# Performance work log

Hardware: AMD Instinct MI355X
Metric: run time of the kernel (lower is better)

## Reference

```python
import jax, jax.numpy as jnp
import numpy as np

# Fixed production-scale sizes (equal-sized graphs so unbatch == reshape)
B, NQ, ND = 64, 32, 512     # graph pairs, query nodes/graph, data nodes/graph
DIN, D, K = 64, 128, 16     # GCN_in_size, GCN_out_size, NTN_k
DEG = 8                     # average degree


def _gcn(x, src, dst, W, b):
    """GCNConv with self loops + symmetric normalization (PyG semantics)."""
    N = x.shape[0]
    loop = jnp.arange(N)
    s = jnp.concatenate([src, loop])
    t = jnp.concatenate([dst, loop])
    deg = jax.ops.segment_sum(jnp.ones_like(t, x.dtype), t, num_segments=N)
    dinv = jnp.where(deg > 0, deg ** -0.5, 0.0)
    norm = (dinv[s] * dinv[t])[:, None]
    h = x @ W
    return jax.ops.segment_sum(h[s] * norm, t, num_segments=N) + b


def _three_gcn(x, ei, W1, b1, W2, b2, W3, b3):
    src, dst = ei[0], ei[1]
    h1 = jax.nn.relu(_gcn(x, src, dst, W1, b1))
    h2 = jax.nn.relu(_gcn(h1, src, dst, W2, b2))
    h3 = jax.nn.relu(_gcn(h2, src, dst, W3, b3))
    return h1, h2, h3


def _level(q, d, Wn, Vn, bn, cw, cb):
    """att_layer + NTN + elementwise mult + 1x1 conv + softmax over data nodes.
    q: [B,NQ,D], d: [B,ND,D] -> (softmaxed map [B,NQ,ND], raw map, he [B,K,NQ,ND])."""
    att = jax.nn.softmax(jnp.einsum('bqd,bnd->bqn', q, d) / jnp.sqrt(jnp.float32(D)), axis=-1)
    qW = jnp.einsum('bqd,kde->bkqe', q, Wn)           # [B,K,NQ,D]
    bil = jnp.einsum('bkqe,bne->bkqn', qW, d)          # [B,K,NQ,ND]
    lq = jnp.einsum('kd,bqd->bkq', Vn[:, :D], q)[:, :, :, None]
    ld = jnp.einsum('kd,bnd->bkn', Vn[:, D:], d)[:, :, None, :]
    he = jax.nn.sigmoid(bil + lq + ld + bn[None, :, None, None]) * att[:, None]
    e_raw = jnp.einsum('k,bkqn->bqn', cw, he) + cb     # 1x1 Conv2d(K->1)
    return jax.nn.softmax(e_raw, axis=-1), e_raw, he


def reference(x_d, edge_index_d, x_q, edge_index_q, batch_index_d, batch_index_q,
              W1, b1, W2, b2, W3, b3,
              Wn1, Vn1, bn1, cw1, cb1,
              Wn2, Vn2, bn2, cw2, cb2,
              Wn3, Vn3, bn3, cw3, cb3,
              w_end, b_end):
    d1, d2, d3 = _three_gcn(x_d, edge_index_d, W1, b1, W2, b2, W3, b3)
    q1, q2, q3 = _three_gcn(x_q, edge_index_q, W1, b1, W2, b2, W3, b3)
    # unbatch: batch indices are sorted with equal graph sizes -> reshape
    d1, d2, d3 = (t.reshape(B, ND, D) for t in (d1, d2, d3))
    q1, q2, q3 = (t.reshape(B, NQ, D) for t in (q1, q2, q3))
    e1, _, he1 = _level(q1, d1, Wn1, Vn1, bn1, cw1, cb1)
    _, e2raw, he2 = _level(q2, d2, Wn2, Vn2, bn2, cw2, cb2)
    e3, _, he3 = _level(q3, d3, Wn3, Vn3, bn3, cw3, cb3)
    # Faithful to source quirks: the zip unpack `e1,e2,e3,h1,h2,h1` rebinds h1 to
    # he_3 (he_1 is never used, he_3 appears twice) and end2 enters the concat
    # PRE-softmax (the softmaxed version was assigned to unused `nd2`).
    stack = jnp.concatenate([e1[:, None], e2raw[:, None], e3[:, None], he3, he2, he3], axis=1)
    out = jnp.einsum('c,bcqn->bqn', w_end, stack) + b_end  # con_end 1x1 conv + squeeze
    return jax.nn.softmax(out, axis=-1)                    # softmax over data nodes


def setup_inputs() -> dict:
    key = jax.random.key(0)
    k = jax.random.split(key, 40)
    n = jax.random.normal
    Nd, Nq = B * ND, B * NQ
    Ed, Eq = Nd * DEG, Nq * DEG
    gid_d = jnp.repeat(jnp.arange(B), ND * DEG)
    gid_q = jnp.repeat(jnp.arange(B), NQ * DEG)
    inp = {
        'x_d': n(k[0], (Nd, DIN), jnp.float32),
        'x_q': n(k[1], (Nq, DIN), jnp.float32),
        'edge_index_d': jnp.stack([jax.random.randint(k[2], (Ed,), 0, ND) + gid_d * ND,
                                   jax.random.randint(k[3], (Ed,), 0, ND) + gid_d * ND]),
        'edge_index_q': jnp.stack([jax.random.randint(k[4], (Eq,), 0, NQ) + gid_q * NQ,
                                   jax.random.randint(k[5], (Eq,), 0, NQ) + gid_q * NQ]),
        'batch_index_d': jnp.repeat(jnp.arange(B), ND),
        'batch_index_q': jnp.repeat(jnp.arange(B), NQ),
        'W1': n(k[6], (DIN, D), jnp.float32) / np.sqrt(DIN), 'b1': jnp.zeros((D,), jnp.float32),
        'W2': n(k[7], (D, D), jnp.float32) / np.sqrt(D), 'b2': jnp.zeros((D,), jnp.float32),
        'W3': n(k[8], (D, D), jnp.float32) / np.sqrt(D), 'b3': jnp.zeros((D,), jnp.float32),
    }
    for i, l in enumerate(('1', '2', '3')):
        inp['Wn' + l] = n(k[10 + 4 * i], (K, D, D), jnp.float32) / np.sqrt(D)
        inp['Vn' + l] = n(k[11 + 4 * i], (K, 2 * D), jnp.float32) / np.sqrt(2 * D)
        inp['bn' + l] = jnp.zeros((K,), jnp.float32)
        inp['cw' + l] = n(k[12 + 4 * i], (K,), jnp.float32) / np.sqrt(K)
        inp['cb' + l] = jnp.zeros((1,), jnp.float32)
    inp['w_end'] = n(k[25], (3 * K + 3,), jnp.float32) / np.sqrt(3 * K + 3)
    inp['b_end'] = jnp.zeros((1,), jnp.float32)
    return inp
```

## Files before the change

### kernel.cpp

```cpp
#include <hip/hip_runtime.h>
#include <math.h>

namespace {
constexpr int cB  = 64;
constexpr int cNQ = 32;
constexpr int cND = 512;
constexpr int cNd = cB * cND;
constexpr int cNq = cB * cNQ;
constexpr int cEd = cNd * 8;
constexpr int cEq = cNq * 8;
constexpr int LD_STRIDE = 516;
constexpr int NB_CVT = 2188, NB_T2BF = 808, NB_CNT = (cEd + cEq) / 256;
constexpr int NB_FILL = (cEd + cEq) / 256;
}

#define F4C(p) (*(const float4*)(p))
#define F4W(p) (*(float4*)(p))

typedef __attribute__((ext_vector_type(8))) __bf16 bf16x8;
typedef __attribute__((ext_vector_type(4))) float floatx4;

__device__ __forceinline__ ushort f2bf(float f) {
  union { float f; unsigned u; } v;
  v.f = f;
  unsigned u = v.u;
  return (ushort)((u + 0x7fffu + ((u >> 16) & 1u)) >> 16);
}
__device__ __forceinline__ float bf2f(ushort u) {
  union { unsigned u; float f; } v;
  v.u = ((unsigned)u) << 16;
  return v.f;
}
__device__ __forceinline__ float4 us4f4(ushort4 u) {
  return make_float4(bf2f(u.x), bf2f(u.y), bf2f(u.z), bf2f(u.w));
}
__device__ __forceinline__ ushort4 f4us4(float4 f) {
  ushort4 o;
  o.x = f2bf(f.x); o.y = f2bf(f.y); o.z = f2bf(f.z); o.w = f2bf(f.w);
  return o;
}
__device__ __forceinline__ float fexp2(float x) {
#if __has_builtin(__builtin_amdgcn_exp2f)
  return __builtin_amdgcn_exp2f(x);
#else
  return exp2f(x);
#endif
}
__device__ __forceinline__ float frcp(float x) {
#if __has_builtin(__builtin_amdgcn_rcpf)
  return __builtin_amdgcn_rcpf(x);
#else
  return 1.0f / x;
#endif
}
__device__ __forceinline__ float fsigmoid(float z) {
  return frcp(1.0f + fexp2(z * -1.4426950408889634f));
}
__device__ __forceinline__ float fexp(float x) { return fexp2(x * 1.4426950408889634f); }

__device__ __forceinline__ int swz_g(int j) { return (((j >> 3) & 7) << 3) | (j & 7); }

__global__ __launch_bounds__(256) void k_front(
    const float* __restrict__ xd, const float* __restrict__ xq,
    const float* __restrict__ v0, const float* __restrict__ v1,
    const float* __restrict__ v2, ushort* __restrict__ oxd, ushort* __restrict__ oxq,
    ushort* __restrict__ ov0, ushort* __restrict__ ov1, ushort* __restrict__ ov2,
    const float* __restrict__ W1, const float* __restrict__ W2,
    const float* __restrict__ W3, const float* __restrict__ Wn0,
    const float* __restrict__ Wn1, const float* __restrict__ Wn2,
    ushort* __restrict__ o1, ushort* __restrict__ o2, ushort* __restrict__ o3,
    ushort* __restrict__ on0, ushort* __restrict__ on1, ushort* __restrict__ on2,
    const int* __restrict__ dst_d, const int* __restrict__ dst_q,
    int* __restrict__ cnt_d, int* __restrict__ cnt_q) {
  __shared__ float tile[32][33];
  int blk = blockIdx.x, tid = threadIdx.x;
  if (blk < NB_CVT) {
    const float* src;
    ushort* dst;
    int i;
    if (blk < 2048) { src = xd; dst = oxd; i = blk * 256 + tid; }
    else if (blk < 2176) { src = xq; dst = oxq; i = (blk - 2048) * 256 + tid; }
    else if (blk < 2180) { src = v0; dst = ov0; i = (blk - 2176) * 256 + tid; }
    else if (blk < 2184) { src = v1; dst = ov1; i = (blk - 2180) * 256 + tid; }
    else { src = v2; dst = ov2; i = (blk - 2184) * 256 + tid; }
    *(ushort4*)(dst + (size_t)i * 4) = f4us4(F4C(src + (size_t)i * 4));
  } else if (blk < NB_CVT + NB_T2BF) {
    int b5 = blk - NB_CVT;
    const float* in;
    ushort* out;
    int R, C, bt, t;
    if (b5 < 8)        { in = W1;  out = o1;  R = 64;  C = 128; bt = 0; t = b5; }
    else if (b5 < 24)  { in = W2;  out = o2;  R = 128; C = 128; bt = 0; t = b5 - 8; }
    else if (b5 < 40)  { in = W3;  out = o3;  R = 128; C = 128; bt = 0; t = b5 - 24; }
    else if (b5 < 296) { in = Wn0; out = on0; R = 128; C = 128; bt = (b5 - 40) >> 4;  t = (b5 - 40) & 15; }
    else if (b5 < 552) { in = Wn1; out = on1; R = 128; C = 128; bt = (b5 - 296) >> 4; t = (b5 - 296) & 15; }
    else               { in = Wn2; out = on2; R = 128; C = 128; bt = (b5 - 552) >> 4; t = (b5 - 552) & 15; }
    int tilesC = C >> 5;
    int tr = t / tilesC, tc = t - tr * tilesC;
    int tx = tid & 31, ty = tid >> 5;
    const float* ib = in + (size_t)bt * R * C;
    ushort* ob = out + (size_t)bt * R * C;
#pragma unroll
    for (int i = 0; i < 4; ++i)
      tile[ty + i * 8][tx] = ib[(tr * 32 + ty + i * 8) * C + tc * 32 + tx];
    __syncthreads();
#pragma unroll
    for (int i = 0; i < 4; ++i)
      ob[(size_t)(tc * 32 + ty + i * 8) * R + tr * 32 + tx] = f2bf(tile[tx][ty + i * 8]);
  } else {
    int i = (blk - NB_CVT - NB_T2BF) * 256 + tid;
    if (i < cEd) atomicAdd(&cnt_d[dst_d[i]], 1);
    else atomicAdd(&cnt_q[dst_q[i - cEd]], 1);
  }
}

__global__ __launch_bounds__(512) void k_scan_dinv(
    const int* __restrict__ cnt_d, const int* __restrict__ cnt_q,
    int* __restrict__ rp_d, int* __restrict__ rp_q,
    float* __restrict__ dinv_d, float* __restrict__ dinv_q) {
  __shared__ int sh[512];
  int blk = blockIdx.x, tid = threadIdx.x;
  if (blk < 64) {
    int v = cnt_d[blk * 512 + tid];
    sh[tid] = v;
    __syncthreads();
    for (int off = 1; off < 512; off <<= 1) {
      int t = (tid >= off) ? sh[tid - off] : 0;
      __syncthreads();
      sh[tid] += t;
      __syncthreads();
    }
    rp_d[blk * 512 + tid] = blk * 4096 + sh[tid] - v;
  } else if (blk < 68) {
    int g = (blk - 64) * 16 + (tid >> 5);
    int lane32 = tid & 31;
    int v = cnt_q[g * 32 + lane32];
    int incl = v;
#pragma unroll
    for (int off = 1; off < 32; off <<= 1) {
      int t = __shfl_up(incl, off, 32);
      if (lane32 >= off) incl += t;
    }
    rp_q[g * 32 + lane32] = g * 256 + incl - v;
  } else {
    int i = (blk - 68) * 512 + tid;
    if (i < cNd) dinv_d[i] = 1.0f / sqrtf((float)(cnt_d[i] + 1));
    else dinv_q[i - cNd] = 1.0f / sqrtf((float)(cnt_q[i - cNd] + 1));
  }
}

__global__ __launch_bounds__(256) void k_fill_gemm1(
    const int* __restrict__ src_d, const int* __restrict__ dst_d,
    const int* __restrict__ src_q, const int* __restrict__ dst_q,
    const int* __restrict__ rp_d, const int* __restrict__ rp_q,
    int* __restrict__ cur_d, int* __restrict__ cur_q, int* __restrict__ col_d,
    int* __restrict__ col_q, const ushort* __restrict__ xdbf,
    const ushort* __restrict__ xqbf, const ushort* __restrict__ w1T,
    const float* __restrict__ dinv_d, const float* __restrict__ dinv_q,
    ushort* __restrict__ htmp) {
  int blk = blockIdx.x, tid = threadIdx.x;
  if (blk < NB_FILL) {
    int i = blk * 256 + tid;
    if (i < cEd) {
      int d = dst_d[i];
      int p = atomicAdd(&cur_d[d], 1);
      col_d[rp_d[d] + p] = src_d[i];
    } else {
      int j = i - cEd;
      int d = dst_q[j];
      int p = atomicAdd(&cur_q[d], 1);
      col_q[rp_q[d] + p] = src_q[j];
    }
    return;
  }
  int blk2 = blk - NB_FILL;
  int wave = tid >> 6, lane = tid & 63;
  int col = lane & 15, quad = lane >> 4;
  bool isQ = blk2 >= 512;
  int node0;
  if (isQ) node0 = (blk2 - 512) * 64;
  else node0 = swz_g(blk2) * 512 + (blk2 >> 6) * 64;
  int mloc = node0 + wave * 16;
  const ushort* X = isQ ? xqbf : xdbf;
  const float* dv = isQ ? dinv_q : dinv_d;
  size_t hbase = isQ ? (size_t)cNd : 0;
  floatx4 acc[8];
#pragma unroll
  for (int ct = 0; ct < 8; ++ct)
#pragma unroll
    for (int r = 0; r < 4; ++r) acc[ct][r] = 0.0f;
#pragma unroll
  for (int kc = 0; kc < 2; ++kc) {
    bf16x8 a = *(const bf16x8*)(X + (size_t)(mloc + col) * 64 + kc * 32 + quad * 8);
#pragma unroll
    for (int ct = 0; ct < 8; ++ct) {
      bf16x8 b = *(const bf16x8*)(w1T + (size_t)(ct * 16 + col) * 64 + kc * 32 + quad * 8);
      acc[ct] = __builtin_amdgcn_mfma_f32_16x16x32_bf16(a, b, acc[ct], 0, 0, 0);
    }
  }
  float sc[4];
#pragma unroll
  for (int r = 0; r < 4; ++r) sc[r] = dv[mloc + quad * 4 + r];
#pragma unroll
  for (int ct = 0; ct < 8; ++ct)
#pragma unroll
    for (int r = 0; r < 4; ++r)
      htmp[(hbase + mloc + quad * 4 + r) * 128 + ct * 16 + col] = f2bf(acc[ct][r] * sc[r]);
}

__global__ __launch_bounds__(256) void gmn_gather_merged(
    const ushort* __restrict__ htmp, const int* __restrict__ rp_d,
    const int* __restrict__ cnt_d, const int* __restrict__ col_d,
    const float* __restrict__ dinv_d, const int* __restrict__ rp_q,
    const int* __restrict__ cnt_q, const int* __restrict__ col_q,
    const float* __restrict__ dinv_q, const float* __restrict__ bias,
    ushort* __restrict__ dbf, ushort* __restrict__ qbf) {
  int blk = blockIdx.x, tid = threadIdx.x;
  bool isQ = blk >= 4096;
  int node;
  if (isQ) {
    int j = blk - 4096;
    node = swz_g(j) * 32 + (j >> 6) * 8 + (tid >> 5);
  } else {
    node = swz_g(blk) * 512 + (blk >> 6) * 8 + (tid >> 5);
  }
  int l = tid & 31;
  const ushort* hs = htmp + (isQ ? (size_t)cNd * 128 : 0);
  const int* rp = isQ ? rp_q : rp_d;
  const int* cnt = isQ ? cnt_q : cnt_d;
  const int* col = isQ ? col_q : col_d;
  const float* dinv = isQ ? dinv_q : dinv_d;
  ushort* outp = isQ ? qbf : dbf;
  int c = cnt[node], s0 = rp[node];
  float dt = dinv[node];
  float4 acc = us4f4(*(const ushort4*)(hs + (size_t)node * 128 + l * 4));
  int cm = c < 32 ? c : 32;
  for (int j0 = 0; j0 < cm; j0 += 8) {
    int ss[8];
    ushort4 v[8];
#pragma unroll
    for (int t = 0; t < 8; ++t) {
      int jj = j0 + t;
      ss[t] = (jj < cm) ? col[s0 + jj] : -1;
    }
#pragma unroll
    for (int t = 0; t < 8; ++t)
      if (ss[t] >= 0) v[t] = *(const ushort4*)(hs + (size_t)ss[t] * 128 + l * 4);
#pragma unroll
    for (int t = 0; t < 8; ++t) {
      if (ss[t] >= 0) {
        float4 f = us4f4(v[t]);
        acc.x += f.x; acc.y += f.y; acc.z += f.z; acc.w += f.w;
      }
    }
  }
  for (int j = 32; j < c; ++j) {
    int s = col[s0 + j];
    float4 f = us4f4(*(const ushort4*)(hs + (size_t)s * 128 + l * 4));
    acc.x += f.x; acc.y += f.y; acc.z += f.z; acc.w += f.w;
  }
  float4 bv = F4C(bias + l * 4);
  float4 r;
  r.x = fmaxf(acc.x * dt + bv.x, 0.0f);
  r.y = fmaxf(acc.y * dt + bv.y, 0.0f);
  r.z = fmaxf(acc.z * dt + bv.z, 0.0f);
  r.w = fmaxf(acc.w * dt + bv.w, 0.0f);
  *(ushort4*)(outp + (size_t)node * 128 + l * 4) = f4us4(r);
}

__global__ __launch_bounds__(256) void gmn_qw(const ushort* __restrict__ qbf,
                                              const ushort* __restrict__ wnT,
                                              ushort* __restrict__ qw) {
  int blk = blockIdx.x, tid = threadIdx.x;
  int wave = tid >> 6, lane = tid & 63;
  int col = lane & 15, quad = lane >> 4;
  int b = swz_g(blk), k = blk >> 6;
  int et0 = wave * 2;
  floatx4 acc[2][2];
#pragma unroll
  for (int qt = 0; qt < 2; ++qt)
#pragma unroll
    for (int ei = 0; ei < 2; ++ei)
#pragma unroll
      for (int r = 0; r < 4; ++r) acc[qt][ei][r] = 0.0f;
#pragma unroll
  for (int kc = 0; kc < 4; ++kc) {
    bf16x8 a0 = *(const bf16x8*)(qbf + (size_t)(b * 32 + col) * 128 + kc * 32 + quad * 8);
    bf16x8 a1 = *(const bf16x8*)(qbf + (size_t)(b * 32 + 16 + col) * 128 + kc * 32 + quad * 8);
#pragma unroll
    for (int ei = 0; ei < 2; ++ei) {
      bf16x8 bf = *(const bf16x8*)(wnT + (size_t)(k * 128 + (et0 + ei) * 16 + col) * 128 +
                                   kc * 32 + quad * 8);
      acc[0][ei] = __builtin_amdgcn_mfma_f32_16x16x32_bf16(a0, bf, acc[0][ei], 0, 0, 0);
      acc[1][ei] = __builtin_amdgcn_mfma_f32_16x16x32_bf16(a1, bf, acc[1][ei], 0, 0, 0);
    }
  }
#pragma unroll
  for (int qt = 0; qt < 2; ++qt)
#pragma unroll
    for (int ei = 0; ei < 2; ++ei)
#pragma unroll
      for (int r = 0; r < 4; ++r)
        qw[((size_t)(b * 16 + k) << 12) + (qt * 16 + quad * 4 + r) * 128 +
           (et0 + ei) * 16 + col] = f2bf(acc[qt][ei][r]);
}

__global__ __launch_bounds__(512, 2) void k_level_gemm(
    const ushort* __restrict__ qbf, const ushort* __restrict__ dbf,
    const ushort* __restrict__ qw, const ushort* __restrict__ vnbf,
    const float* __restrict__ bn, const float* __restrict__ cw,
    const float* __restrict__ w_end, const float* __restrict__ b_end,
    int o1, int o2, int hasF, int do_sm, int mode, int widx,
    float* __restrict__ accb, float* __restrict__ out,
    const ushort* __restrict__ gWT, const float* __restrict__ dinv_d,
    const float* __restrict__ dinv_q, ushort* __restrict__ htmp) {
  __shared__ float s_ld[16 * LD_STRIDE];
  __shared__ float s_lq[16 * 16];
  __shared__ float s_red[16 * 8];
  int tid = threadIdx.x;
  int wave = tid >> 6, lane = tid & 63;
  int col = lane & 15, quad = lane >> 4;

  if (blockIdx.x >= 128) {
    int gblk = blockIdx.x - 128;
    bool isQ = gblk >= 256;
    int node0;
    if (isQ) node0 = (gblk - 256) * 128;
    else node0 = swz_g(gblk) * 512 + (gblk >> 6) * 128;
    int mloc = node0 + wave * 16;
    const ushort* X = isQ ? qbf : dbf;
    const float* dv = isQ ? dinv_q : dinv_d;
    size_t hbase = isQ ? (size_t)cNd : 0;
    floatx4 acc[8];
#pragma unroll
    for (int ct = 0; ct < 8; ++ct)
#pragma unroll
      for (int r = 0; r < 4; ++r) acc[ct][r] = 0.0f;
#pragma unroll
    for (int kc = 0; kc < 4; ++kc) {
      bf16x8 a = *(const bf16x8*)(X + (size_t)(mloc + col) * 128 + kc * 32 + quad * 8);
#pragma unroll
      for (int ct = 0; ct < 8; ++ct) {
        bf16x8 b = *(const bf16x8*)(gWT + (size_t)(ct * 16 + col) * 128 + kc * 32 + quad * 8);
        acc[ct] = __builtin_amdgcn_mfma_f32_16x16x32_bf16(a, b, acc[ct], 0, 0, 0);
      }
    }
    float sc[4];
#pragma unroll
    for (int r = 0; r < 4; ++r) sc[r] = dv[mloc + quad * 4 + r];
#pragma unroll
    for (int ct = 0; ct < 8; ++ct)
#pragma unroll
      for (int r = 0; r < 4; ++r)
        htmp[(hbase + mloc + quad * 4 + r) * 128 + ct * 16 + col] = f2bf(acc[ct][r] * sc[r]);
    return;
  }

  int b = swz_g(blockIdx.x & 63);
  int qh = blockIdx.x >> 6;
  int n0 = wave * 64;

  bf16x8 bfr[4][4];
#pragma unroll
  for (int s = 0; s < 4; ++s)
#pragma unroll
    for (int kc = 0; kc < 4; ++kc)
      bfr[s][kc] = *(const bf16x8*)(dbf + ((size_t)(b * 512 + n0 + s * 16 + col) << 7) +
                                    kc * 32 + quad * 8);
  bf16x8 aq[4];
#pragma unroll
  for (int kc = 0; kc < 4; ++kc)
    aq[kc] = *(const bf16x8*)(qbf + (size_t)(b * 32 + qh * 16 + col) * 128 +
                              kc * 32 + quad * 8);

  floatx4 att[4];
#pragma unroll
  for (int s = 0; s < 4; ++s)
#pragma unroll
    for (int r = 0; r < 4; ++r) att[s][r] = 0.0f;
#pragma unroll
  for (int kc = 0; kc < 4; ++kc)
#pragma unroll
    for (int s = 0; s < 4; ++s)
      att[s] = __builtin_amdgcn_mfma_f32_16x16x32_bf16(aq[kc], bfr[s][kc], att[s], 0, 0, 0);
  const float sc = 0.088388347648318440550f;
#pragma unroll
  for (int s = 0; s < 4; ++s)
#pragma unroll
    for (int r = 0; r < 4; ++r) att[s][r] *= sc;

  {
    bf16x8 vn2[4];
#pragma unroll
    for (int kc = 0; kc < 4; ++kc)
      vn2[kc] = *(const bf16x8*)(vnbf + col * 256 + 128 + kc * 32 + quad * 8);
#pragma unroll
    for (int s = 0; s < 4; ++s) {
      floatx4 lda;
#pragma unroll
      for (int r = 0; r < 4; ++r) lda[r] = 0.0f;
#pragma unroll
      for (int kc = 0; kc < 4; ++kc)
        lda = __builtin_amdgcn_mfma_f32_16x16x32_bf16(bfr[s][kc], vn2[kc], lda, 0, 0, 0);
#pragma unroll
      for (int r = 0; r < 4; ++r)
        s_ld[col * LD_STRIDE + n0 + s * 16 + quad * 4 + r] = lda[r];
    }
  }
  if (wave == 0) {
    bf16x8 vn1[4];
#pragma unroll
    for (int kc = 0; kc < 4; ++kc)
      vn1[kc] = *(const bf16x8*)(vnbf + col * 256 + kc * 32 + quad * 8);
    floatx4 lqa;
#pragma unroll
    for (int r = 0; r < 4; ++r) lqa[r] = 0.0f;
#pragma unroll
    for (int kc = 0; kc < 4; ++kc)
      lqa = __builtin_amdgcn_mfma_f32_16x16x32_bf16(aq[kc], vn1[kc], lqa, 0, 0, 0);
#pragma unroll
    for (int r = 0; r < 4; ++r) s_lq[col * 16 + quad * 4 + r] = lqa[r];
  }
  __syncthreads();

  float red[4], M[4];
#pragma unroll
  for (int r = 0; r < 4; ++r) {
    float m = fmaxf(fmaxf(att[0][r], att[1][r]), fmaxf(att[2][r], att[3][r]));
#pragma unroll
    for (int o = 1; o < 16; o <<= 1) m = fmaxf(m, __shfl_xor(m, o, 64));
    red[r] = m;
  }
  if (col == 0)
#pragma unroll
    for (int r = 0; r < 4; ++r) s_red[(quad * 4 + r) * 8 + wave] = red[r];
  __syncthreads();
#pragma unroll
  for (int r = 0; r < 4; ++r) {
    float m = s_red[(quad * 4 + r) * 8];
#pragma unroll
    for (int w = 1; w < 8; ++w) m = fmaxf(m, s_red[(quad * 4 + r) * 8 + w]);
    M[r] = m;
  }
  __syncthreads();
#pragma unroll
  for (int s = 0; s < 4; ++s)
#pragma unroll
    for (int r = 0; r < 4; ++r) att[s][r] = fexp(att[s][r] - M[r]);
#pragma unroll
  for (int r = 0; r < 4; ++r) {
    float m = att[0][r] + att[1][r] + att[2][r] + att[3][r];
#pragma unroll
    for (int o = 1; o < 16; o <<= 1) m += __shfl_xor(m, o, 64);
    red[r] = m;
  }
  if (col == 0)
#pragma unroll
    for (int r = 0; r < 4; ++r) s_red[(quad * 4 + r) * 8 + wave] = red[r];
  __syncthreads();
#pragma unroll
  for (int r = 0; r < 4; ++r) {
    float m = s_red[(quad * 4 + r) * 8];
#pragma unroll
    for (int w = 1; w < 8; ++w) m += s_red[(quad * 4 + r) * 8 + w];
    M[r] = frcp(m);
  }
  __syncthreads();
#pragma unroll
  for (int s = 0; s < 4; ++s)
#pragma unroll
    for (int r = 0; r < 4; ++r) att[s][r] *= M[r];

  floatx4 eacc[4], facc[4];
#pragma unroll
  for (int s = 0; s < 4; ++s)
#pragma unroll
    for (int r = 0; r < 4; ++r) { eacc[s][r] = 0.0f; facc[s][r] = 0.0f; }

#pragma unroll 4
  for (int k = 0; k < 16; ++k) {
    const ushort* qk = qw + ((size_t)(b * 16 + k) << 12) + (qh * 16 + col) * 128 + quad * 8;
    bf16x8 a0 = *(const bf16x8*)(qk);
    bf16x8 a1 = *(const bf16x8*)(qk + 32);
    bf16x8 a2 = *(const bf16x8*)(qk + 64);
    bf16x8 a3 = *(const bf16x8*)(qk + 96);
    floatx4 bil[4];
#pragma unroll
    for (int s = 0; s < 4; ++s) {
#pragma unroll
      for (int r = 0; r < 4; ++r) bil[s][r] = 0.0f;
      bil[s] = __builtin_amdgcn_mfma_f32_16x16x32_bf16(a0, bfr[s][0], bil[s], 0, 0, 0);
      bil[s] = __builtin_amdgcn_mfma_f32_16x16x32_bf16(a1, bfr[s][1], bil[s], 0, 0, 0);
      bil[s] = __builtin_amdgcn_mfma_f32_16x16x32_bf16(a2, bfr[s][2], bil[s], 0, 0, 0);
      bil[s] = __builtin_amdgcn_mfma_f32_16x16x32_bf16(a3, bfr[s][3], bil[s], 0, 0, 0);
    }
    float bnk = bn[k], cwk = cw[k];
    float wkk = 0.0f;
    if (hasF) {
      wkk = w_end[o1 + k];
      if (o2 >= 0) wkk += w_end[o2 + k];
    }
    float lqv[4];
#pragma unroll
    for (int r = 0; r < 4; ++r) lqv[r] = s_lq[k * 16 + quad * 4 + r] + bnk;
#pragma unroll
    for (int s = 0; s < 4; ++s) {
      float ldv = s_ld[k * LD_STRIDE + n0 + s * 16 + col];
#pragma unroll
      for (int r = 0; r < 4; ++r) {
        float sg = fsigmoid(bil[s][r] + lqv[r] + ldv);
        eacc[s][r] += cwk * sg;
        facc[s][r] += wkk * sg;
      }
    }
  }

#pragma unroll
  for (int s = 0; s < 4; ++s)
#pragma unroll
    for (int r = 0; r < 4; ++r) {
      eacc[s][r] *= att[s][r];
      facc[s][r] *= att[s][r];
    }
  if (do_sm) {
#pragma unroll
    for (int r = 0; r < 4; ++r) {
      float m = fmaxf(fmaxf(eacc[0][r], eacc[1][r]), fmaxf(eacc[2][r], eacc[3][r]));
#pragma unroll
      for (int o = 1; o < 16; o <<= 1) m = fmaxf(m, __shfl_xor(m, o, 64));
      red[r] = m;
    }
    if (col == 0)
#pragma unroll
      for (int r = 0; r < 4; ++r) s_red[(quad * 4 + r) * 8 + wave] = red[r];
    __syncthreads();
#pragma unroll
    for (int r = 0; r < 4; ++r) {
      float m = s_red[(quad * 4 + r) * 8];
#pragma unroll
      for (int w = 1; w < 8; ++w) m = fmaxf(m, s_red[(quad * 4 + r) * 8 + w]);
      M[r] = m;
    }
    __syncthreads();
#pragma unroll
    for (int s = 0; s < 4; ++s)
#pragma unroll
      for (int r = 0; r < 4; ++r) eacc[s][r] = fexp(eacc[s][r] - M[r]);
#pragma unroll
    for (int r = 0; r < 4; ++r) {
      float m = eacc[0][r] + eacc[1][r] + eacc[2][r] + eacc[3][r];
#pragma unroll
      for (int o = 1; o < 16; o <<= 1) m += __shfl_xor(m, o, 64);
      red[r] = m;
    }
    if (col == 0)
#pragma unroll
      for (int r = 0; r < 4; ++r) s_red[(quad * 4 + r) * 8 + wave] = red[r];
    __syncthreads();
#pragma unroll
    for (int r = 0; r < 4; ++r) {
      float m = s_red[(quad * 4 + r) * 8];
#pragma unroll
      for (int w = 1; w < 8; ++w) m += s_red[(quad * 4 + r) * 8 + w];
      M[r] = frcp(m);
    }
    __syncthreads();
#pragma unroll
    for (int s = 0; s < 4; ++s)
#pragma unroll
      for (int r = 0; r < 4; ++r) eacc[s][r] *= M[r];
  }
  float w = w_end[widx];
#pragma unroll
  for (int s = 0; s < 4; ++s)
#pragma unroll
    for (int r = 0; r < 4; ++r) eacc[s][r] = w * eacc[s][r] + (hasF ? facc[s][r] : 0.0f);

  if (mode == 0) {
#pragma unroll
    for (int s = 0; s < 4; ++s)
#pragma unroll
      for (int r = 0; r < 4; ++r)
        accb[((size_t)(b * 32 + qh * 16 + quad * 4 + r) << 9) + n0 + s * 16 + col] =
            eacc[s][r];
  } else if (mode == 1) {
#pragma unroll
    for (int s = 0; s < 4; ++s)
#pragma unroll
      for (int r = 0; r < 4; ++r)
        accb[((size_t)(b * 32 + qh * 16 + quad * 4 + r) << 9) + n0 + s * 16 + col] +=
            eacc[s][r];
  } else {
    float be = b_end[0];
#pragma unroll
    for (int s = 0; s < 4; ++s)
#pragma unroll
      for (int r = 0; r < 4; ++r)
        eacc[s][r] += accb[((size_t)(b * 32 + qh * 16 + quad * 4 + r) << 9) +
                           n0 + s * 16 + col] + be;
#pragma unroll
    for (int r = 0; r < 4; ++r) {
      float m = fmaxf(fmaxf(eacc[0][r], eacc[1][r]), fmaxf(eacc[2][r], eacc[3][r]));
#pragma unroll
      for (int o = 1; o < 16; o <<= 1) m = fmaxf(m, __shfl_xor(m, o, 64));
      red[r] = m;
    }
    if (col == 0)
#pragma unroll
      for (int r = 0; r < 4; ++r) s_red[(quad * 4 + r) * 8 + wave] = red[r];
    __syncthreads();
#pragma unroll
    for (int r = 0; r < 4; ++r) {
      float m = s_red[(quad * 4 + r) * 8];
#pragma unroll
      for (int w2 = 1; w2 < 8; ++w2) m = fmaxf(m, s_red[(quad * 4 + r) * 8 + w2]);
      M[r] = m;
    }
    __syncthreads();
#pragma unroll
    for (int s = 0; s < 4; ++s)
#pragma unroll
      for (int r = 0; r < 4; ++r) eacc[s][r] = fexp(eacc[s][r] - M[r]);
#pragma unroll
    for (int r = 0; r < 4; ++r) {
      float m = eacc[0][r] + eacc[1][r] + eacc[2][r] + eacc[3][r];
#pragma unroll
      for (int o = 1; o < 16; o <<= 1) m += __shfl_xor(m, o, 64);
      red[r] = m;
    }
    if (col == 0)
#pragma unroll
      for (int r = 0; r < 4; ++r) s_red[(quad * 4 + r) * 8 + wave] = red[r];
    __syncthreads();
#pragma unroll
    for (int r = 0; r < 4; ++r) {
      float m = s_red[(quad * 4 + r) * 8];
#pragma unroll
      for (int w2 = 1; w2 < 8; ++w2) m += s_red[(quad * 4 + r) * 8 + w2];
      M[r] = frcp(m);
    }
#pragma unroll
    for (int s = 0; s < 4; ++s)
#pragma unroll
      for (int r = 0; r < 4; ++r)
        out[((size_t)(b * 32 + qh * 16 + quad * 4 + r) << 9) + n0 + s * 16 + col] =
            eacc[s][r] * M[r];
  }
}

extern "C" void kernel_launch(void* const* d_in, const int* in_sizes, int n_in,
                              void* d_out, int out_size, void* d_ws, size_t ws_size,
                              hipStream_t stream) {
  (void)in_sizes; (void)n_in; (void)out_size; (void)ws_size;
  const float* x_d = (const float*)d_in[0];
  const float* x_q = (const float*)d_in[1];
  const int* ei_d = (const int*)d_in[2];
  const int* ei_q = (const int*)d_in[3];
  const float* W1 = (const float*)d_in[6];
  const float* b1 = (const float*)d_in[7];
  const float* W2 = (const float*)d_in[8];
  const float* b2 = (const float*)d_in[9];
  const float* W3 = (const float*)d_in[10];
  const float* b3 = (const float*)d_in[11];
  const float* Wn[3] = {(const float*)d_in[12], (const float*)d_in[17], (const float*)d_in[22]};
  const float* Vn[3] = {(const float*)d_in[13], (const float*)d_in[18], (const float*)d_in[23]};
  const float* bn[3] = {(const float*)d_in[14], (const float*)d_in[19], (const float*)d_in[24]};
  const float* cw[3] = {(const float*)d_in[15], (const float*)d_in[20], (const float*)d_in[25]};
  const float* w_end = (const float*)d_in[27];
  const float* b_end = (const float*)d_in[28];
  float* out = (float*)d_out;

  char* wsp = (char*)d_ws;
  auto alloc = [&](size_t nbytes) {
    void* p = (void*)wsp;
    wsp += (nbytes + 255) & ~(size_t)255;
    return p;
  };
  int* cnt_d = (int*)alloc(cNd * 4);
  int* cnt_q = (int*)alloc(cNq * 4);
  int* cur_d = (int*)alloc(cNd * 4);
  int* cur_q = (int*)alloc(cNq * 4);
  float* dinv_d = (float*)alloc(cNd * 4);
  float* dinv_q = (float*)alloc(cNq * 4);
  int* rp_d = (int*)alloc(cNd * 4);
  int* rp_q = (int*)alloc(cNq * 4);
  int* col_d = (int*)alloc((size_t)cEd * 4);
  int* col_q = (int*)alloc((size_t)cEq * 4);
  ushort* xdbf = (ushort*)alloc((size_t)cNd * 64 * 2);
  ushort* xqbf = (ushort*)alloc((size_t)cNq * 64 * 2);
  ushort* w1T = (ushort*)alloc(128 * 64 * 2);
  ushort* w2T = (ushort*)alloc(128 * 128 * 2);
  ushort* w3T = (ushort*)alloc(128 * 128 * 2);
  ushort* wnT[3];
  for (int l = 0; l < 3; ++l) wnT[l] = (ushort*)alloc((size_t)16 * 128 * 128 * 2);
  ushort* vnbf[3];
  for (int l = 0; l < 3; ++l) vnbf[l] = (ushort*)alloc(16 * 256 * 2);
  ushort* htmp = (ushort*)alloc((size_t)(cNd + cNq) * 128 * 2);
  ushort* dbf = (ushort*)alloc((size_t)cNd * 128 * 2);
  ushort* qbf[3];
  for (int l = 0; l < 3; ++l) qbf[l] = (ushort*)alloc((size_t)cNq * 128 * 2);
  float* accb = (float*)alloc((size_t)cB * cNQ * cND * 4);
  ushort* qwbuf = (ushort*)alloc((size_t)cB * 16 * 32 * 128 * 2);

  const int* src_d = ei_d;
  const int* dst_d = ei_d + cEd;
  const int* src_q = ei_q;
  const int* dst_q = ei_q + cEq;

  hipMemsetAsync(cnt_d, 0, (size_t)2 * (cNd + cNq) * 4, stream);

  k_front<<<NB_CVT + NB_T2BF + NB_CNT, 256, 0, stream>>>(
      x_d, x_q, Vn[0], Vn[1], Vn[2], xdbf, xqbf, vnbf[0], vnbf[1], vnbf[2], W1, W2,
      W3, Wn[0], Wn[1], Wn[2], w1T, w2T, w3T, wnT[0], wnT[1], wnT[2], dst_d, dst_q,
      cnt_d, cnt_q);

  k_scan_dinv<<<136, 512, 0, stream>>>(cnt_d, cnt_q, rp_d, rp_q, dinv_d, dinv_q);

  k_fill_gemm1<<<NB_FILL + 544, 256, 0, stream>>>(
      src_d, dst_d, src_q, dst_q, rp_d, rp_q, cur_d, cur_q, col_d, col_q, xdbf, xqbf,
      w1T, dinv_d, dinv_q, htmp);

  const float* bias[3] = {b1, b2, b3};
  const ushort* nextWT[3] = {w2T, w3T, nullptr};
  const int o1s[3] = {0, 19, 3};
  const int o2s[3] = {-1, -1, 35};
  const int hasF[3] = {0, 1, 1};
  const int dosms[3] = {1, 0, 1};
  const int modes[3] = {0, 1, 2};

  for (int l = 0; l < 3; ++l) {
    gmn_gather_merged<<<(cNd + cNq) / 8, 256, 0, stream>>>(
        htmp, rp_d, cnt_d, col_d, dinv_d, rp_q, cnt_q, col_q, dinv_q, bias[l], dbf,
        qbf[l]);
    gmn_qw<<<1024, 256, 0, stream>>>(qbf[l], wnT[l], qwbuf);
    int grid = (l < 2) ? (128 + 272) : 128;
    k_level_gemm<<<grid, 512, 0, stream>>>(
        qbf[l], dbf, qwbuf, vnbf[l], bn[l], cw[l], w_end, b_end, o1s[l], o2s[l],
        hasF[l], dosms[l], modes[l], l, accb, out, nextWT[l], dinv_d, dinv_q, htmp);
  }
}
```

Baseline: 300.2 us.

## Build per-graph CSR in shared memory and fuse query gather with QW GEMM

CSR construction (count, scan, dinv, fill) now runs per graph inside the front kernel using shared-memory atomics. This drops the memset, the scan kernel and the global-atomic fill pass, and gemm1 becomes its own kernel. Per level, the query-node gather is merged into the qW GEMM: each block aggregates one graph's 32 query nodes into swizzled LDS and multiplies them against all K Wn slices, which removes one launch per level. The cost is that the QW work runs on only 64 blocks, each doing 16 K-slices serially, so parallelism drops.

```diff
diff --git a/kernel.cpp b/kernel.cpp
--- a/kernel.cpp
+++ b/kernel.cpp
@@ -10,8 +10,9 @@
 constexpr int cEd = cNd * 8;
 constexpr int cEq = cNq * 8;
 constexpr int LD_STRIDE = 516;
-constexpr int NB_CVT = 2188, NB_T2BF = 808, NB_CNT = (cEd + cEq) / 256;
-constexpr int NB_FILL = (cEd + cEq) / 256;
+constexpr int NB_CVT = 2188, NB_T2BF = 808;
+constexpr int NB_CSRD = 64;
+constexpr int NB_CSRQ = 8;
 }
 
 #define F4C(p) (*(const float4*)(p))
@@ -60,7 +61,7 @@
 
 __device__ __forceinline__ int swz_g(int j) { return (((j >> 3) & 7) << 3) | (j & 7); }
 
-__global__ __launch_bounds__(256) void k_front(
+__global__ __launch_bounds__(256) void k_front_csr(
     const float* __restrict__ xd, const float* __restrict__ xq,
     const float* __restrict__ v0, const float* __restrict__ v1,
     const float* __restrict__ v2, ushort* __restrict__ oxd, ushort* __restrict__ oxq,
@@ -70,9 +71,16 @@
     const float* __restrict__ Wn1, const float* __restrict__ Wn2,
     ushort* __restrict__ o1, ushort* __restrict__ o2, ushort* __restrict__ o3,
     ushort* __restrict__ on0, ushort* __restrict__ on1, ushort* __restrict__ on2,
-    const int* __restrict__ dst_d, const int* __restrict__ dst_q,
-    int* __restrict__ cnt_d, int* __restrict__ cnt_q) {
+    const int* __restrict__ src_d, const int* __restrict__ dst_d,
+    const int* __restrict__ src_q, const int* __restrict__ dst_q,
+    int* __restrict__ cnt_d, int* __restrict__ cnt_q,
+    int* __restrict__ rp_d, int* __restrict__ rp_q,
+    float* __restrict__ dinv_d, float* __restrict__ dinv_q,
+    int* __restrict__ col_d, int* __restrict__ col_q) {
   __shared__ float tile[32][33];
+  __shared__ int s_cnt[512];
+  __shared__ int s_base[512];
+  __shared__ int s_cur[512];
   int blk = blockIdx.x, tid = threadIdx.x;
   if (blk < NB_CVT) {
     const float* src;
@@ -107,73 +115,82 @@
 #pragma unroll
     for (int i = 0; i < 4; ++i)
       ob[(size_t)(tc * 32 + ty + i * 8) * R + tr * 32 + tx] = f2bf(tile[tx][ty + i * 8]);
+  } else if (blk < NB_CVT + NB_T2BF + NB_CSRD) {
+    int g = blk - (NB_CVT + NB_T2BF);
+    const int* dstg = dst_d + g * 4096;
+    const int* srcg = src_d + g * 4096;
+    int nbase = g * 512;
+    s_cnt[tid] = 0; s_cnt[tid + 256] = 0;
+    __syncthreads();
+    for (int e = tid; e < 4096; e += 256) atomicAdd(&s_cnt[dstg[e] - nbase], 1);
+    __syncthreads();
+    int c0 = s_cnt[tid], c1 = s_cnt[tid + 256];
+    s_base[tid] = c0; s_base[tid + 256] = c1;
+    __syncthreads();
+    for (int off = 1; off < 512; off <<= 1) {
+      int a = (tid >= off) ? s_base[tid - off] : 0;
+      int b = (tid + 256 >= off) ? s_base[tid + 256 - off] : 0;
+      __syncthreads();
+      s_base[tid] += a; s_base[tid + 256] += b;
+      __syncthreads();
+    }
+    int e0 = s_base[tid] - c0, e1 = s_base[tid + 256] - c1;
+    s_base[tid] = e0; s_base[tid + 256] = e1;
+    s_cur[tid] = 0; s_cur[tid + 256] = 0;
+    cnt_d[nbase + tid] = c0;
+    cnt_d[nbase + tid + 256] = c1;
+    rp_d[nbase + tid] = g * 4096 + e0;
+    rp_d[nbase + tid + 256] = g * 4096 + e1;
+    dinv_d[nbase + tid] = 1.0f / sqrtf((float)(c0 + 1));
+    dinv_d[nbase + tid + 256] = 1.0f / sqrtf((float)(c1 + 1));
+    __syncthreads();
+    for (int e = tid; e < 4096; e += 256) {
+      int d = dstg[e] - nbase;
+      int p = atomicAdd(&s_cur[d], 1);
+      col_d[g * 4096 + s_base[d] + p] = srcg[e];
+    }
   } else {
-    int i = (blk - NB_CVT - NB_T2BF) * 256 + tid;
-    if (i < cEd) atomicAdd(&cnt_d[dst_d[i]], 1);
-    else atomicAdd(&cnt_q[dst_q[i - cEd]], 1);
-  }
-}
-
-__global__ __launch_bounds__(512) void k_scan_dinv(
-    const int* __restrict__ cnt_d, const int* __restrict__ cnt_q,
-    int* __restrict__ rp_d, int* __restrict__ rp_q,
-    float* __restrict__ dinv_d, float* __restrict__ dinv_q) {
-  __shared__ int sh[512];
-  int blk = blockIdx.x, tid = threadIdx.x;
-  if (blk < 64) {
-    int v = cnt_d[blk * 512 + tid];
-    sh[tid] = v;
-    __syncthreads();
-    for (int off = 1; off < 512; off <<= 1) {
-      int t = (tid >= off) ? sh[tid - off] : 0;
-      __syncthreads();
-      sh[tid] += t;
-      __syncthreads();
-    }
-    rp_d[blk * 512 + tid] = blk * 4096 + sh[tid] - v;
-  } else if (blk < 68) {
-    int g = (blk - 64) * 16 + (tid >> 5);
-    int lane32 = tid & 31;
-    int v = cnt_q[g * 32 + lane32];
+    int qb = blk - (NB_CVT + NB_T2BF + NB_CSRD);
+    int lg = tid >> 5, lane32 = tid & 31;
+    int g = qb * 8 + lg;
+    const int* dstg = dst_q + g * 256;
+    const int* srcg = src_q + g * 256;
+    int nbase = g * 32;
+    s_cnt[tid] = 0;
+    __syncthreads();
+#pragma unroll
+    for (int j = 0; j < 8; ++j)
+      atomicAdd(&s_cnt[lg * 32 + (dstg[lane32 + j * 32] - nbase)], 1);
+    __syncthreads();
+    int v = s_cnt[tid];
     int incl = v;
 #pragma unroll
     for (int off = 1; off < 32; off <<= 1) {
       int t = __shfl_up(incl, off, 32);
       if (lane32 >= off) incl += t;
     }
-    rp_q[g * 32 + lane32] = g * 256 + incl - v;
-  } else {
-    int i = (blk - 68) * 512 + tid;
-    if (i < cNd) dinv_d[i] = 1.0f / sqrtf((float)(cnt_d[i] + 1));
-    else dinv_q[i - cNd] = 1.0f / sqrtf((float)(cnt_q[i - cNd] + 1));
-  }
-}
-
-__global__ __launch_bounds__(256) void k_fill_gemm1(
-    const int* __restrict__ src_d, const int* __restrict__ dst_d,
-    const int* __restrict__ src_q, const int* __restrict__ dst_q,
-    const int* __restrict__ rp_d, const int* __restrict__ rp_q,
-    int* __restrict__ cur_d, int* __restrict__ cur_q, int* __restrict__ col_d,
-    int* __restrict__ col_q, const ushort* __restrict__ xdbf,
-    const ushort* __restrict__ xqbf, const ushort* __restrict__ w1T,
-    const float* __restrict__ dinv_d, const float* __restrict__ dinv_q,
-    ushort* __restrict__ htmp) {
-  int blk = blockIdx.x, tid = threadIdx.x;
-  if (blk < NB_FILL) {
-    int i = blk * 256 + tid;
-    if (i < cEd) {
-      int d = dst_d[i];
-      int p = atomicAdd(&cur_d[d], 1);
-      col_d[rp_d[d] + p] = src_d[i];
-    } else {
-      int j = i - cEd;
-      int d = dst_q[j];
-      int p = atomicAdd(&cur_q[d], 1);
-      col_q[rp_q[d] + p] = src_q[j];
-    }
-    return;
-  }
-  int blk2 = blk - NB_FILL;
+    int excl = incl - v;
+    cnt_q[nbase + lane32] = v;
+    rp_q[nbase + lane32] = g * 256 + excl;
+    dinv_q[nbase + lane32] = 1.0f / sqrtf((float)(v + 1));
+    s_base[tid] = excl;
+    s_cur[tid] = 0;
+    __syncthreads();
+#pragma unroll
+    for (int j = 0; j < 8; ++j) {
+      int e = lane32 + j * 32;
+      int d = dstg[e] - nbase;
+      int p = atomicAdd(&s_cur[lg * 32 + d], 1);
+      col_q[g * 256 + s_base[lg * 32 + d] + p] = srcg[e];
+    }
+  }
+}
+
+__global__ __launch_bounds__(256) void k_gemm1(
+    const ushort* __restrict__ xdbf, const ushort* __restrict__ xqbf,
+    const ushort* __restrict__ w1T, const float* __restrict__ dinv_d,
+    const float* __restrict__ dinv_q, ushort* __restrict__ htmp) {
+  int blk2 = blockIdx.x, tid = threadIdx.x;
   int wave = tid >> 6, lane = tid & 63;
   int col = lane & 15, quad = lane >> 4;
   bool isQ = blk2 >= 512;
@@ -208,101 +225,140 @@
       htmp[(hbase + mloc + quad * 4 + r) * 128 + ct * 16 + col] = f2bf(acc[ct][r] * sc[r]);
 }
 
-__global__ __launch_bounds__(256) void gmn_gather_merged(
+__global__ __launch_bounds__(256) void k_gather_qw(
     const ushort* __restrict__ htmp, const int* __restrict__ rp_d,
     const int* __restrict__ cnt_d, const int* __restrict__ col_d,
     const float* __restrict__ dinv_d, const int* __restrict__ rp_q,
     const int* __restrict__ cnt_q, const int* __restrict__ col_q,
     const float* __restrict__ dinv_q, const float* __restrict__ bias,
-    ushort* __restrict__ dbf, ushort* __restrict__ qbf) {
+    ushort* __restrict__ dbf, ushort* __restrict__ qbf,
+    const ushort* __restrict__ wnT, ushort* __restrict__ qw) {
+  __shared__ ushort q_s[32 * 128];
   int blk = blockIdx.x, tid = threadIdx.x;
-  bool isQ = blk >= 4096;
-  int node;
-  if (isQ) {
-    int j = blk - 4096;
-    node = swz_g(j) * 32 + (j >> 6) * 8 + (tid >> 5);
-  } else {
-    node = swz_g(blk) * 512 + (blk >> 6) * 8 + (tid >> 5);
-  }
-  int l = tid & 31;
-  const ushort* hs = htmp + (isQ ? (size_t)cNd * 128 : 0);
-  const int* rp = isQ ? rp_q : rp_d;
-  const int* cnt = isQ ? cnt_q : cnt_d;
-  const int* col = isQ ? col_q : col_d;
-  const float* dinv = isQ ? dinv_q : dinv_d;
-  ushort* outp = isQ ? qbf : dbf;
-  int c = cnt[node], s0 = rp[node];
-  float dt = dinv[node];
-  float4 acc = us4f4(*(const ushort4*)(hs + (size_t)node * 128 + l * 4));
-  int cm = c < 32 ? c : 32;
-  for (int j0 = 0; j0 < cm; j0 += 8) {
-    int ss[8];
-    ushort4 v[8];
-#pragma unroll
-    for (int t = 0; t < 8; ++t) {
-      int jj = j0 + t;
-      ss[t] = (jj < cm) ? col[s0 + jj] : -1;
-    }
-#pragma unroll
-    for (int t = 0; t < 8; ++t)
-      if (ss[t] >= 0) v[t] = *(const ushort4*)(hs + (size_t)ss[t] * 128 + l * 4);
-#pragma unroll
-    for (int t = 0; t < 8; ++t) {
-      if (ss[t] >= 0) {
-        float4 f = us4f4(v[t]);
-        acc.x += f.x; acc.y += f.y; acc.z += f.z; acc.w += f.w;
+  if (blk >= 64) {
+    int j = blk - 64;
+    int node = swz_g(j) * 512 + (j >> 6) * 8 + (tid >> 5);
+    int l = tid & 31;
+    int c = cnt_d[node], s0 = rp_d[node];
+    float dt = dinv_d[node];
+    float4 acc = us4f4(*(const ushort4*)(htmp + (size_t)node * 128 + l * 4));
+    int cm = c < 32 ? c : 32;
+    for (int j0 = 0; j0 < cm; j0 += 8) {
+      int ss[8];
+      ushort4 v[8];
+#pragma unroll
+      for (int t = 0; t < 8; ++t) {
+        int jj = j0 + t;
+        ss[t] = (jj < cm) ? col_d[s0 + jj] : -1;
       }
-    }
-  }
-  for (int j = 32; j < c; ++j) {
-    int s = col[s0 + j];
-    float4 f = us4f4(*(const ushort4*)(hs + (size_t)s * 128 + l * 4));
-    acc.x += f.x; acc.y += f.y; acc.z += f.z; acc.w += f.w;
-  }
-  float4 bv = F4C(bias + l * 4);
-  float4 r;
-  r.x = fmaxf(acc.x * dt + bv.x, 0.0f);
-  r.y = fmaxf(acc.y * dt + bv.y, 0.0f);
-  r.z = fmaxf(acc.z * dt + bv.z, 0.0f);
-  r.w = fmaxf(acc.w * dt + bv.w, 0.0f);
-  *(ushort4*)(outp + (size_t)node * 128 + l * 4) = f4us4(r);
-}
-
-__global__ __launch_bounds__(256) void gmn_qw(const ushort* __restrict__ qbf,
-                                              const ushort* __restrict__ wnT,
-                                              ushort* __restrict__ qw) {
-  int blk = blockIdx.x, tid = threadIdx.x;
+#pragma unroll
+      for (int t = 0; t < 8; ++t)
+        if (ss[t] >= 0) v[t] = *(const ushort4*)(htmp + (size_t)ss[t] * 128 + l * 4);
+#pragma unroll
+      for (int t = 0; t < 8; ++t) {
+        if (ss[t] >= 0) {
+          float4 f = us4f4(v[t]);
+          acc.x += f.x; acc.y += f.y; acc.z += f.z; acc.w += f.w;
+        }
+      }
+    }
+    for (int j2 = 32; j2 < c; ++j2) {
+      int s = col_d[s0 + j2];
+      float4 f = us4f4(*(const ushort4*)(htmp + (size_t)s * 128 + l * 4));
+      acc.x += f.x; acc.y += f.y; acc.z += f.z; acc.w += f.w;
+    }
+    float4 bv = F4C(bias + l * 4);
+    float4 r;
+    r.x = fmaxf(acc.x * dt + bv.x, 0.0f);
+    r.y = fmaxf(acc.y * dt + bv.y, 0.0f);
+    r.z = fmaxf(acc.z * dt + bv.z, 0.0f);
+    r.w = fmaxf(acc.w * dt + bv.w, 0.0f);
+    *(ushort4*)(dbf + (size_t)node * 128 + l * 4) = f4us4(r);
+    return;
+  }
+  int b = blk;
+  {
+    int n = tid >> 3, seg = tid & 7, d0 = seg * 16;
+    int node = b * 32 + n;
+    int c = cnt_q[node], s0 = rp_q[node];
+    float dt = dinv_q[node];
+    const ushort* hq = htmp + (size_t)cNd * 128;
+    const ushort* own = hq + (size_t)node * 128 + d0;
+    float4 a0 = us4f4(*(const ushort4*)(own));
+    float4 a1 = us4f4(*(const ushort4*)(own + 4));
+    float4 a2 = us4f4(*(const ushort4*)(own + 8));
+    float4 a3 = us4f4(*(const ushort4*)(own + 12));
+    for (int j2 = 0; j2 < c; ++j2) {
+      int s = col_q[s0 + j2];
+      const ushort* rr = hq + (size_t)s * 128 + d0;
+      float4 f0 = us4f4(*(const ushort4*)(rr));
+      float4 f1 = us4f4(*(const ushort4*)(rr + 4));
+      float4 f2 = us4f4(*(const ushort4*)(rr + 8));
+      float4 f3 = us4f4(*(const ushort4*)(rr + 12));
+      a0.x += f0.x; a0.y += f0.y; a0.z += f0.z; a0.w += f0.w;
+      a1.x += f1.x; a1.y += f1.y; a1.z += f1.z; a1.w += f1.w;
+      a2.x += f2.x; a2.y += f2.y; a2.z += f2.z; a2.w += f2.w;
+      a3.x += f3.x; a3.y += f3.y; a3.z += f3.z; a3.w += f3.w;
+    }
+    float4 bv0 = F4C(bias + d0), bv1 = F4C(bias + d0 + 4);
+    float4 bv2 = F4C(bias + d0 + 8), bv3 = F4C(bias + d0 + 12);
+    float4 r0, r1, r2, r3;
+    r0.x = fmaxf(a0.x * dt + bv0.x, 0.0f); r0.y = fmaxf(a0.y * dt + bv0.y, 0.0f);
+    r0.z = fmaxf(a0.z * dt + bv0.z, 0.0f); r0.w = fmaxf(a0.w * dt + bv0.w, 0.0f);
+    r1.x = fmaxf(a1.x * dt + bv1.x, 0.0f); r1.y = fmaxf(a1.y * dt + bv1.y, 0.0f);
+    r1.z = fmaxf(a1.z * dt + bv1.z, 0.0f); r1.w = fmaxf(a1.w * dt + bv1.w, 0.0f);
+    r2.x = fmaxf(a2.x * dt + bv2.x, 0.0f); r2.y = fmaxf(a2.y * dt + bv2.y, 0.0f);
+    r2.z = fmaxf(a2.z * dt + bv2.z, 0.0f); r2.w = fmaxf(a2.w * dt + bv2.w, 0.0f);
+    r3.x = fmaxf(a3.x * dt + bv3.x, 0.0f); r3.y = fmaxf(a3.y * dt + bv3.y, 0.0f);
+    r3.z = fmaxf(a3.z * dt + bv3.z, 0.0f); r3.w = fmaxf(a3.w * dt + bv3.w, 0.0f);
+    ushort4 u0 = f4us4(r0), u1 = f4us4(r1), u2 = f4us4(r2), u3 = f4us4(r3);
+    *(ushort4*)(qbf + (size_t)node * 128 + d0) = u0;
+    *(ushort4*)(qbf + (size_t)node * 128 + d0 + 4) = u1;
+    *(ushort4*)(qbf + (size_t)node * 128 + d0 + 8) = u2;
+    *(ushort4*)(qbf + (size_t)node * 128 + d0 + 12) = u3;
+    char* qsb = (char*)q_s;
+    int x0 = (n * 256 + d0 * 2) ^ ((n & 7) << 4);
+    int x1 = (n * 256 + d0 * 2 + 16) ^ ((n & 7) << 4);
+    *(ushort4*)(qsb + x0) = u0;
+    *(ushort4*)(qsb + x0 + 8) = u1;
+    *(ushort4*)(qsb + x1) = u2;
+    *(ushort4*)(qsb + x1 + 8) = u3;
+  }
+  __syncthreads();
   int wave = tid >> 6, lane = tid & 63;
   int col = lane & 15, quad = lane >> 4;
-  int b = swz_g(blk), k = blk >> 6;
-  int et0 = wave * 2;
-  floatx4 acc[2][2];
-#pragma unroll
-  for (int qt = 0; qt < 2; ++qt)
-#pragma unroll
-    for (int ei = 0; ei < 2; ++ei)
-#pragma unroll
-      for (int r = 0; r < 4; ++r) acc[qt][ei][r] = 0.0f;
-#pragma unroll
-  for (int kc = 0; kc < 4; ++kc) {
-    bf16x8 a0 = *(const bf16x8*)(qbf + (size_t)(b * 32 + col) * 128 + kc * 32 + quad * 8);
-    bf16x8 a1 = *(const bf16x8*)(qbf + (size_t)(b * 32 + 16 + col) * 128 + kc * 32 + quad * 8);
-#pragma unroll
-    for (int ei = 0; ei < 2; ++ei) {
-      bf16x8 bf = *(const bf16x8*)(wnT + (size_t)(k * 128 + (et0 + ei) * 16 + col) * 128 +
-                                   kc * 32 + quad * 8);
-      acc[0][ei] = __builtin_amdgcn_mfma_f32_16x16x32_bf16(a0, bf, acc[0][ei], 0, 0, 0);
-      acc[1][ei] = __builtin_amdgcn_mfma_f32_16x16x32_bf16(a1, bf, acc[1][ei], 0, 0, 0);
-    }
-  }
-#pragma unroll
-  for (int qt = 0; qt < 2; ++qt)
-#pragma unroll
-    for (int ei = 0; ei < 2; ++ei)
-#pragma unroll
-      for (int r = 0; r < 4; ++r)
-        qw[((size_t)(b * 16 + k) << 12) + (qt * 16 + quad * 4 + r) * 128 +
-           (et0 + ei) * 16 + col] = f2bf(acc[qt][ei][r]);
+  const char* qsb = (const char*)q_s;
+  for (int kk = 0; kk < 4; ++kk) {
+    int k = wave * 4 + kk;
+    floatx4 acc[2][8];
+#pragma unroll
+    for (int qt = 0; qt < 2; ++qt)
+#pragma unroll
+      for (int et = 0; et < 8; ++et)
+#pragma unroll
+        for (int r = 0; r < 4; ++r) acc[qt][et][r] = 0.0f;
+#pragma unroll
+    for (int kc = 0; kc < 4; ++kc) {
+      int r0 = col, r1 = 16 + col;
+      bf16x8 a0 = *(const bf16x8*)(qsb + ((r0 * 256 + kc * 64 + quad * 16) ^ ((r0 & 7) << 4)));
+      bf16x8 a1 = *(const bf16x8*)(qsb + ((r1 * 256 + kc * 64 + quad * 16) ^ ((r1 & 7) << 4)));
+#pragma unroll
+      for (int et = 0; et < 8; ++et) {
+        bf16x8 bb = *(const bf16x8*)(wnT + (size_t)(k * 128 + et * 16 + col) * 128 +
+                                     kc * 32 + quad * 8);
+        acc[0][et] = __builtin_amdgcn_mfma_f32_16x16x32_bf16(a0, bb, acc[0][et], 0, 0, 0);
+        acc[1][et] = __builtin_amdgcn_mfma_f32_16x16x32_bf16(a1, bb, acc[1][et], 0, 0, 0);
+      }
+    }
+#pragma unroll
+    for (int qt = 0; qt < 2; ++qt)
+#pragma unroll
+      for (int et = 0; et < 8; ++et)
+#pragma unroll
+        for (int r = 0; r < 4; ++r)
+          qw[((size_t)(b * 16 + k) << 12) + (qt * 16 + quad * 4 + r) * 128 +
+             et * 16 + col] = f2bf(acc[qt][et][r]);
+  }
 }
 
 __global__ __launch_bounds__(512, 2) void k_level_gemm(
@@ -678,8 +734,6 @@
   };
   int* cnt_d = (int*)alloc(cNd * 4);
   int* cnt_q = (int*)alloc(cNq * 4);
-  int* cur_d = (int*)alloc(cNd * 4);
-  int* cur_q = (int*)alloc(cNq * 4);
   float* dinv_d = (float*)alloc(cNd * 4);
   float* dinv_q = (float*)alloc(cNq * 4);
   int* rp_d = (int*)alloc(cNd * 4);
@@ -707,18 +761,13 @@
   const int* src_q = ei_q;
   const int* dst_q = ei_q + cEq;
 
-  hipMemsetAsync(cnt_d, 0, (size_t)2 * (cNd + cNq) * 4, stream);
-
-  k_front<<<NB_CVT + NB_T2BF + NB_CNT, 256, 0, stream>>>(
+  k_front_csr<<<NB_CVT + NB_T2BF + NB_CSRD + NB_CSRQ, 256, 0, stream>>>(
       x_d, x_q, Vn[0], Vn[1], Vn[2], xdbf, xqbf, vnbf[0], vnbf[1], vnbf[2], W1, W2,
-      W3, Wn[0], Wn[1], Wn[2], w1T, w2T, w3T, wnT[0], wnT[1], wnT[2], dst_d, dst_q,
-      cnt_d, cnt_q);
-
-  k_scan_dinv<<<136, 512, 0, stream>>>(cnt_d, cnt_q, rp_d, rp_q, dinv_d, dinv_q);
-
-  k_fill_gemm1<<<NB_FILL + 544, 256, 0, stream>>>(
-      src_d, dst_d, src_q, dst_q, rp_d, rp_q, cur_d, cur_q, col_d, col_q, xdbf, xqbf,
-      w1T, dinv_d, dinv_q, htmp);
+      W3, Wn[0], Wn[1], Wn[2], w1T, w2T, w3T, wnT[0], wnT[1], wnT[2],
+      src_d, dst_d, src_q, dst_q, cnt_d, cnt_q, rp_d, rp_q, dinv_d, dinv_q,
+      col_d, col_q);
+
+  k_gemm1<<<544, 256, 0, stream>>>(xdbf, xqbf, w1T, dinv_d, dinv_q, htmp);
 
   const float* bias[3] = {b1, b2, b3};
   const ushort* nextWT[3] = {w2T, w3T, nullptr};
@@ -729,10 +778,9 @@
   const int modes[3] = {0, 1, 2};
 
   for (int l = 0; l < 3; ++l) {
-    gmn_gather_merged<<<(cNd + cNq) / 8, 256, 0, stream>>>(
+    k_gather_qw<<<64 + cNd / 8, 256, 0, stream>>>(
         htmp, rp_d, cnt_d, col_d, dinv_d, rp_q, cnt_q, col_q, dinv_q, bias[l], dbf,
-        qbf[l]);
-    gmn_qw<<<1024, 256, 0, stream>>>(qbf[l], wnT[l], qwbuf);
+        qbf[l], wnT[l], qwbuf);
     int grid = (l < 2) ? (128 + 272) : 128;
     k_level_gemm<<<grid, 512, 0, stream>>>(
         qbf[l], dbf, qwbuf, vnbf[l], bn[l], cw[l], w_end, b_end, o1s[l], o2s[l],
```

Result: slower. 338.0 us (+12.6%).
